# Optimization experiments

Measured on AMD Instinct MI355X. Metric: run time of the kernel, lower is better.

The kernel has to match this reference:

```python
import jax, jax.numpy as jnp
import numpy as np

SEGMENT_LENGTHS = [2048, 4096, 8192]
DILATION_RATES = [1, 2, 4]
RING_SIZE = 4


def _head_groups(h, g):
    base, rem = divmod(h, g)
    return [base + (1 if i < rem else 0) for i in range(g)]


def _dilation_pattern(n, seg, r, group_idx):
    # Per-segment dilated index pattern of total length n (index_select target).
    s = min(seg, n)
    off = group_idx % r
    base = (off + np.arange(0, s, r)) % s          # stride-r indices within segment
    pat_seg = np.tile(base, r)[:s]                  # repeat to fill segment length
    nseg = n // s
    pat = (pat_seg[None, :] + np.arange(nseg)[:, None] * s).reshape(-1)
    return pat


def _apply_dilation(x):
    # x: (b, n, h, d). Gather along sequence per head group.
    b, n, h, d = x.shape
    groups = _head_groups(h, len(SEGMENT_LENGTHS))
    outs, hs = [], 0
    for i, (seg, r, g) in enumerate(zip(SEGMENT_LENGTHS, DILATION_RATES, groups)):
        if g == 0:
            continue
        pat = jnp.asarray(_dilation_pattern(n, seg, r, i))
        outs.append(x[:, pat, hs:hs + g, :])
        hs += g
    return jnp.concatenate(outs, axis=2)


def setup_inputs() -> dict:
    key = jax.random.key(0)
    k1, k2, k3 = jax.random.split(key, 3)
    shape = (1, 8192, 16, 64)
    return {
        "q": jax.random.normal(k1, shape, dtype=jnp.float32),
        "k": jax.random.normal(k2, shape, dtype=jnp.float32),
        "v": jax.random.normal(k3, shape, dtype=jnp.float32),
    }


def reference(q, k, v):
    b, n, h, d = q.shape
    scale = 1.0 / jnp.sqrt(jnp.asarray(d, q.dtype))
    chunk = n // RING_SIZE

    # Dilate queries once; dilate each local KV chunk (ring-distributed layout).
    qt = _apply_dilation(q).transpose(0, 2, 1, 3)   # (b, h, n, d)

    acc_out = jnp.zeros((b, h, n, d), q.dtype)
    acc_lse = jnp.full((b, h, n), -jnp.inf, q.dtype)

    # Simulated ring pass: iterate over KV chunks with online-LSE accumulation.
    for c in range(RING_SIZE):
        kc = _apply_dilation(k[:, c * chunk:(c + 1) * chunk])  # (b, chunk, h, d)
        vc = _apply_dilation(v[:, c * chunk:(c + 1) * chunk])
        scores = jnp.einsum('bhqd,bkhd->bhqk', qt, kc) * scale
        lse_c = jax.nn.logsumexp(scores, axis=-1)              # (b, h, n)
        out_c = jnp.einsum('bhqk,bkhd->bhqd',
                           jax.nn.softmax(scores, axis=-1), vc)
        new_lse = jnp.logaddexp(acc_lse, lse_c)
        w_old = jnp.exp(acc_lse - new_lse)[..., None]
        w_new = jnp.exp(lse_c - new_lse)[..., None]
        acc_out = w_old * acc_out + w_new * out_c
        acc_lse = new_lse

    return acc_out.transpose(0, 2, 1, 3)  # (b, n, h, d)
```

## Files before the change

### kernel.cpp

```cpp
#include <hip/hip_runtime.h>
#include <hip/hip_bf16.h>
#include <math.h>

typedef __attribute__((ext_vector_type(4))) float f32x4;
typedef __attribute__((ext_vector_type(8))) short bf16x8;
typedef __attribute__((ext_vector_type(4))) short s16x4;

#define NH 16
#define HD 64
#define BM 128
#define BN 64
#define WM 32
#define LDS_K 72
#define TILE_B 18432
#define TILE_S 9216
#define WS_NEEDED 23003136ull

__device__ __forceinline__ short f2bf(float f) {
    union { float f; unsigned u; } x; x.f = f;
    unsigned r = x.u + 0x7fffu + ((x.u >> 16) & 1u);
    return (short)(r >> 16);
}
__device__ __forceinline__ unsigned pack2bf(float a, float b) {
    union { float f; unsigned u; } x, y; x.f = a; y.f = b;
    return __builtin_amdgcn_perm(y.u + 0x8000u, x.u + 0x8000u, 0x07060302u);
}
__device__ __forceinline__ float elem(const float4& r, int j) {
    return ((const float*)&r)[j];
}
__device__ __forceinline__ size_t head_base(int h) {
    if (h < 6)  return (size_t)h * (128 * TILE_B);
    if (h < 11) return 6ull * (128 * TILE_B) + (size_t)(h - 6) * (64 * TILE_B);
    return 6ull * (128 * TILE_B) + 5ull * (64 * TILE_B) + (size_t)(h - 11) * (32 * TILE_B);
}

__global__ __launch_bounds__(256)
void rda_pack(const float* __restrict__ K, const float* __restrict__ V, char* __restrict__ W) {
    int bid = blockIdx.x;
    int h, t, type;
    if (bid < 768)       { type = 0; h = bid >> 7;                t = bid & 127; }
    else if (bid < 1088) { type = 1; h = 6 + ((bid - 768) >> 6);  t = (bid - 768) & 63; }
    else                 { type = 2; h = 11 + ((bid - 1088) >> 5); t = (bid - 1088) & 31; }
    int rate = 1 << type, off = type;
    char* tile = W + head_base(h) + (size_t)t * TILE_B;
    int tid = threadIdx.x;
    {
        int row = tid >> 2, c = (tid & 3) * 16;
        int pos = rate * (t * 64 + row) + off;
        const float* p = K + ((size_t)pos * NH + h) * HD + c;
        float4 a0 = ((const float4*)p)[0], a1 = ((const float4*)p)[1];
        float4 a2 = ((const float4*)p)[2], a3 = ((const float4*)p)[3];
        uint4 d0, d1;
        d0.x = pack2bf(elem(a0,0), elem(a0,1)); d0.y = pack2bf(elem(a0,2), elem(a0,3));
        d0.z = pack2bf(elem(a1,0), elem(a1,1)); d0.w = pack2bf(elem(a1,2), elem(a1,3));
        d1.x = pack2bf(elem(a2,0), elem(a2,1)); d1.y = pack2bf(elem(a2,2), elem(a2,3));
        d1.z = pack2bf(elem(a3,0), elem(a3,1)); d1.w = pack2bf(elem(a3,2), elem(a3,3));
        char* dst = tile + row * (LDS_K * 2) + c * 2;
        ((uint4*)dst)[0] = d0;
        ((uint4*)dst)[1] = d1;
    }
    {
        int vr = (tid & 15) * 4, vc = (tid >> 4) * 4;
        float4 vv[4];
#pragma unroll
        for (int i = 0; i < 4; ++i) {
            int pos = rate * (t * 64 + vr + i) + off;
            vv[i] = *(const float4*)(V + ((size_t)pos * NH + h) * HD + vc);
        }
#pragma unroll
        for (int j = 0; j < 4; ++j) {
            uint2 w;
            w.x = pack2bf(elem(vv[0], j), elem(vv[1], j));
            w.y = pack2bf(elem(vv[2], j), elem(vv[3], j));
            *(uint2*)(tile + 9216 + (vc + j) * (LDS_K * 2) + vr * 2) = w;
        }
    }
}

__global__ __launch_bounds__(256, 3)
void rda_attn(const float* __restrict__ Q, const char* __restrict__ W, float* __restrict__ O) {
    __shared__ __align__(16) short sKV[2 * TILE_S];
    __shared__ __align__(16) short sP[4][WM * 64];

    int bid = blockIdx.x;
    int h, mb, type;
    if (bid < 384)      { type = 0; h = bid >> 6;               mb = bid & 63; }
    else if (bid < 544) { type = 1; h = 6 + ((bid - 384) >> 5); mb = (bid - 384) & 31; }
    else                { type = 2; h = 11 + ((bid - 544) >> 4); mb = (bid - 544) & 15; }
    int rate = 1 << type;
    int off  = type;
    int nsteps = 128 >> type;

    int tid  = threadIdx.x;
    int wave = tid >> 6;
    int lane = tid & 63;
    int ln   = lane & 15;
    int quad = lane >> 4;

    const float SC = 0.125f * 1.4426950408889634f;

    int qbase = mb * BM + wave * WM;
    bf16x8 qf[2][2];
#pragma unroll
    for (int mt = 0; mt < 2; ++mt) {
        int u = qbase + mt * 16 + ln;
        size_t base = ((size_t)(rate * u + off) * NH + h) * HD;
#pragma unroll
        for (int ks = 0; ks < 2; ++ks) {
            const float* p = Q + base + ks * 32 + quad * 8;
            float4 a = ((const float4*)p)[0];
            float4 b = ((const float4*)p)[1];
            union { uint4 u4; bf16x8 f; } cv;
            cv.u4.x = pack2bf(elem(a,0)*SC, elem(a,1)*SC);
            cv.u4.y = pack2bf(elem(a,2)*SC, elem(a,3)*SC);
            cv.u4.z = pack2bf(elem(b,0)*SC, elem(b,1)*SC);
            cv.u4.w = pack2bf(elem(b,2)*SC, elem(b,3)*SC);
            qf[mt][ks] = cv.f;
        }
    }

    f32x4 acc[2][4];
#pragma unroll
    for (int mt = 0; mt < 2; ++mt)
#pragma unroll
        for (int dt = 0; dt < 4; ++dt) acc[mt][dt] = (f32x4){0.f, 0.f, 0.f, 0.f};
    float lp[2] = {0.f, 0.f};

    const char* gh = W + head_base(h);

    auto stage = [&](const char* gt, int lB) {
#pragma unroll
        for (int r = 0; r < 4; ++r) {
            int c = r * 4096 + tid * 16;
            __builtin_amdgcn_global_load_lds(
                (const __attribute__((address_space(1))) unsigned*)(gt + c),
                (__attribute__((address_space(3))) unsigned*)((char*)sKV + lB + c),
                16, 0, 0);
        }
        if (tid < 128) {
            int c = 16384 + tid * 16;
            __builtin_amdgcn_global_load_lds(
                (const __attribute__((address_space(1))) unsigned*)(gt + c),
                (__attribute__((address_space(3))) unsigned*)((char*)sKV + lB + c),
                16, 0, 0);
        }
    };

    stage(gh, 0);
    int pB = 0;

    char* pbase = (char*)&sP[wave][0];

    for (int kb = 0; kb < nsteps; ++kb) {
        __syncthreads();

        if (kb + 1 < nsteps) stage(gh + (size_t)(kb + 1) * TILE_B, pB ^ TILE_B);

        const short* sK  = (const short*)((const char*)sKV + pB);
        const short* sVT = sK + BN * LDS_K;

        f32x4 st[4][2];
        __builtin_amdgcn_s_setprio(1);
#pragma unroll
        for (int kt = 0; kt < 4; ++kt) {
            bf16x8 a0 = *(bf16x8*)&sK[(kt * 16 + ln) * LDS_K + quad * 8];
            bf16x8 a1 = *(bf16x8*)&sK[(kt * 16 + ln) * LDS_K + 32 + quad * 8];
#pragma unroll
            for (int mt = 0; mt < 2; ++mt) {
                f32x4 c = (f32x4){0.f, 0.f, 0.f, 0.f};
                c = __builtin_amdgcn_mfma_f32_16x16x32_bf16(a0, qf[mt][0], c, 0, 0, 0);
                c = __builtin_amdgcn_mfma_f32_16x16x32_bf16(a1, qf[mt][1], c, 0, 0, 0);
                st[kt][mt] = c;
            }
        }
        __builtin_amdgcn_s_setprio(0);

#pragma unroll
        for (int mt = 0; mt < 2; ++mt)
#pragma unroll
            for (int kt = 0; kt < 4; ++kt) {
                float p0 = __builtin_amdgcn_exp2f(st[kt][mt][0]);
                float p1 = __builtin_amdgcn_exp2f(st[kt][mt][1]);
                float p2 = __builtin_amdgcn_exp2f(st[kt][mt][2]);
                float p3 = __builtin_amdgcn_exp2f(st[kt][mt][3]);
                st[kt][mt][0] = p0; st[kt][mt][1] = p1;
                st[kt][mt][2] = p2; st[kt][mt][3] = p3;
                lp[mt] += (p0 + p1) + (p2 + p3);
            }

#pragma unroll
        for (int mt = 0; mt < 2; ++mt)
#pragma unroll
            for (int kt = 0; kt < 4; ++kt) {
                uint2 pk;
                pk.x = pack2bf(st[kt][mt][0], st[kt][mt][1]);
                pk.y = pack2bf(st[kt][mt][2], st[kt][mt][3]);
                int prow = mt * 16 + ln;
                int pbyte = (prow * 128 + (kt * 16 + quad * 4) * 2) ^ ((prow & 7) << 4);
                *(uint2*)(pbase + pbyte) = pk;
            }
        __asm__ volatile("s_waitcnt lgkmcnt(0)" ::: "memory");

        __builtin_amdgcn_s_setprio(1);
#pragma unroll
        for (int ksk = 0; ksk < 2; ++ksk) {
            int b0 = (ln * 128 + (ksk * 32 + quad * 8) * 2) ^ ((ln & 7) << 4);
            int b1 = ((16 + ln) * 128 + (ksk * 32 + quad * 8) * 2) ^ ((ln & 7) << 4);
            bf16x8 pa0 = *(bf16x8*)(pbase + b0);
            bf16x8 pa1 = *(bf16x8*)(pbase + b1);
#pragma unroll
            for (int dt = 0; dt < 4; ++dt) {
                bf16x8 vb = *(bf16x8*)&sVT[(dt * 16 + ln) * LDS_K + ksk * 32 + quad * 8];
                acc[0][dt] = __builtin_amdgcn_mfma_f32_16x16x32_bf16(pa0, vb, acc[0][dt], 0, 0, 0);
                acc[1][dt] = __builtin_amdgcn_mfma_f32_16x16x32_bf16(pa1, vb, acc[1][dt], 0, 0, 0);
            }
        }
        __builtin_amdgcn_s_setprio(0);
        pB ^= TILE_B;
    }

#pragma unroll
    for (int mt = 0; mt < 2; ++mt) {
        lp[mt] += __shfl_xor(lp[mt], 16);
        lp[mt] += __shfl_xor(lp[mt], 32);
#pragma unroll
        for (int r = 0; r < 4; ++r) {
            float lO = __shfl(lp[mt], quad * 4 + r);
            float inv = 1.0f / lO;
            int u = qbase + mt * 16 + quad * 4 + r;
#pragma unroll
            for (int dt = 0; dt < 4; ++dt) {
                float val = acc[mt][dt][r] * inv;
                int dcol = dt * 16 + ln;
                if (type == 0) {
                    O[((size_t)u * NH + h) * HD + dcol] = val;
                } else if (type == 1) {
                    int r0 = ((u >> 11) << 12) + (u & 2047);
                    O[((size_t)r0 * NH + h) * HD + dcol] = val;
                    O[((size_t)(r0 + 2048) * NH + h) * HD + dcol] = val;
                } else {
#pragma unroll
                    for (int t = 0; t < 4; ++t)
                        O[((size_t)(u + t * 2048) * NH + h) * HD + dcol] = val;
                }
            }
        }
    }
}

__global__ __launch_bounds__(256, 2)
void rda_attn_fb(const float* __restrict__ Q, const float* __restrict__ K,
                 const float* __restrict__ V, float* __restrict__ O) {
    __shared__ short sK[BN * LDS_K];
    __shared__ short sVT[HD * LDS_K];
    __shared__ short sP[4][WM * LDS_K];

    int bid = blockIdx.x;
    int h, mb, type;
    if (bid < 384)      { type = 0; h = bid >> 6;               mb = bid & 63; }
    else if (bid < 544) { type = 1; h = 6 + ((bid - 384) >> 5); mb = (bid - 384) & 31; }
    else                { type = 2; h = 11 + ((bid - 544) >> 4); mb = (bid - 544) & 15; }
    int rate = 1 << type;
    int off  = type;
    int nsteps = 128 >> type;

    int tid  = threadIdx.x;
    int wave = tid >> 6;
    int lane = tid & 63;
    int ln   = lane & 15;
    int quad = lane >> 4;

    const float SC = 0.125f * 1.4426950408889634f;

    int qbase = mb * BM + wave * WM;
    bf16x8 qf[2][2];
#pragma unroll
    for (int mt = 0; mt < 2; ++mt) {
        int u = qbase + mt * 16 + ln;
        size_t base = ((size_t)(rate * u + off) * NH + h) * HD;
#pragma unroll
        for (int ks = 0; ks < 2; ++ks) {
            const float* p = Q + base + ks * 32 + quad * 8;
            float4 a = ((const float4*)p)[0];
            float4 b = ((const float4*)p)[1];
            bf16x8 f;
#pragma unroll
            for (int i = 0; i < 4; ++i) { f[i] = f2bf(elem(a, i) * SC); f[4 + i] = f2bf(elem(b, i) * SC); }
            qf[mt][ks] = f;
        }
    }

    f32x4 acc[2][4];
#pragma unroll
    for (int mt = 0; mt < 2; ++mt)
#pragma unroll
        for (int dt = 0; dt < 4; ++dt) acc[mt][dt] = (f32x4){0.f, 0.f, 0.f, 0.f};
    float m_i[2] = {-INFINITY, -INFINITY};
    float l_i[2] = {0.f, 0.f};

    int srow = tid >> 2, sc0 = (tid & 3) * 16;
    int vr = (tid >> 4) * 4, vc = (tid & 15) * 4;

    for (int kb = 0; kb < nsteps; ++kb) {
        {
            int kpos = rate * (kb * BN + srow) + off;
            const float* p = K + ((size_t)kpos * NH + h) * HD + sc0;
            float4 kv0 = ((const float4*)p)[0], kv1 = ((const float4*)p)[1];
            float4 kv2 = ((const float4*)p)[2], kv3 = ((const float4*)p)[3];
            bf16x8 f0, f1;
#pragma unroll
            for (int i = 0; i < 4; ++i) {
                f0[i] = f2bf(elem(kv0, i)); f0[4 + i] = f2bf(elem(kv1, i));
                f1[i] = f2bf(elem(kv2, i)); f1[4 + i] = f2bf(elem(kv3, i));
            }
            *(bf16x8*)&sK[srow * LDS_K + sc0] = f0;
            *(bf16x8*)&sK[srow * LDS_K + sc0 + 8] = f1;
        }
        {
            float4 vv[4];
#pragma unroll
            for (int i = 0; i < 4; ++i) {
                int kpos = rate * (kb * BN + vr + i) + off;
                vv[i] = *(const float4*)(V + ((size_t)kpos * NH + h) * HD + vc);
            }
#pragma unroll
            for (int j = 0; j < 4; ++j) {
                s16x4 t;
                t[0] = f2bf(elem(vv[0], j)); t[1] = f2bf(elem(vv[1], j));
                t[2] = f2bf(elem(vv[2], j)); t[3] = f2bf(elem(vv[3], j));
                *(s16x4*)&sVT[(vc + j) * LDS_K + vr] = t;
            }
        }
        __syncthreads();

        f32x4 st[4][2];
#pragma unroll
        for (int kt = 0; kt < 4; ++kt) {
            bf16x8 a0 = *(bf16x8*)&sK[(kt * 16 + ln) * LDS_K + quad * 8];
            bf16x8 a1 = *(bf16x8*)&sK[(kt * 16 + ln) * LDS_K + 32 + quad * 8];
#pragma unroll
            for (int mt = 0; mt < 2; ++mt) {
                f32x4 c = (f32x4){0.f, 0.f, 0.f, 0.f};
                c = __builtin_amdgcn_mfma_f32_16x16x32_bf16(a0, qf[mt][0], c, 0, 0, 0);
                c = __builtin_amdgcn_mfma_f32_16x16x32_bf16(a1, qf[mt][1], c, 0, 0, 0);
                st[kt][mt] = c;
            }
        }

#pragma unroll
        for (int mt = 0; mt < 2; ++mt) {
            float tmax = -INFINITY;
#pragma unroll
            for (int kt = 0; kt < 4; ++kt)
#pragma unroll
                for (int r = 0; r < 4; ++r) tmax = fmaxf(tmax, st[kt][mt][r]);
            tmax = fmaxf(tmax, __shfl_xor(tmax, 16));
            tmax = fmaxf(tmax, __shfl_xor(tmax, 32));
            float mnew = fmaxf(m_i[mt], tmax);
            float al = exp2f(m_i[mt] - mnew);
            m_i[mt] = mnew;
            float rs = 0.f;
#pragma unroll
            for (int kt = 0; kt < 4; ++kt)
#pragma unroll
                for (int r = 0; r < 4; ++r) {
                    float pe = exp2f(st[kt][mt][r] - mnew);
                    st[kt][mt][r] = pe;
                    rs += pe;
                }
            rs += __shfl_xor(rs, 16);
            rs += __shfl_xor(rs, 32);
            l_i[mt] = l_i[mt] * al + rs;
#pragma unroll
            for (int r = 0; r < 4; ++r) {
                float aO = __shfl(al, quad * 4 + r);
#pragma unroll
                for (int dt = 0; dt < 4; ++dt) acc[mt][dt][r] *= aO;
            }
        }

#pragma unroll
        for (int mt = 0; mt < 2; ++mt)
#pragma unroll
            for (int kt = 0; kt < 4; ++kt) {
                s16x4 pk;
                pk[0] = f2bf(st[kt][mt][0]); pk[1] = f2bf(st[kt][mt][1]);
                pk[2] = f2bf(st[kt][mt][2]); pk[3] = f2bf(st[kt][mt][3]);
                *(s16x4*)&sP[wave][(mt * 16 + ln) * LDS_K + kt * 16 + quad * 4] = pk;
            }
        __asm__ volatile("s_waitcnt lgkmcnt(0)" ::: "memory");

#pragma unroll
        for (int ksk = 0; ksk < 2; ++ksk) {
            bf16x8 pa0 = *(bf16x8*)&sP[wave][(ln) * LDS_K + ksk * 32 + quad * 8];
            bf16x8 pa1 = *(bf16x8*)&sP[wave][(16 + ln) * LDS_K + ksk * 32 + quad * 8];
#pragma unroll
            for (int dt = 0; dt < 4; ++dt) {
                bf16x8 vb = *(bf16x8*)&sVT[(dt * 16 + ln) * LDS_K + ksk * 32 + quad * 8];
                acc[0][dt] = __builtin_amdgcn_mfma_f32_16x16x32_bf16(pa0, vb, acc[0][dt], 0, 0, 0);
                acc[1][dt] = __builtin_amdgcn_mfma_f32_16x16x32_bf16(pa1, vb, acc[1][dt], 0, 0, 0);
            }
        }
        __syncthreads();
    }

#pragma unroll
    for (int mt = 0; mt < 2; ++mt) {
#pragma unroll
        for (int r = 0; r < 4; ++r) {
            float lO = __shfl(l_i[mt], quad * 4 + r);
            float inv = 1.0f / lO;
            int u = qbase + mt * 16 + quad * 4 + r;
#pragma unroll
            for (int dt = 0; dt < 4; ++dt) {
                float val = acc[mt][dt][r] * inv;
                int dcol = dt * 16 + ln;
                if (type == 0) {
                    O[((size_t)u * NH + h) * HD + dcol] = val;
                } else if (type == 1) {
                    int r0 = ((u >> 11) << 12) + (u & 2047);
                    O[((size_t)r0 * NH + h) * HD + dcol] = val;
                    O[((size_t)(r0 + 2048) * NH + h) * HD + dcol] = val;
                } else {
#pragma unroll
                    for (int t = 0; t < 4; ++t)
                        O[((size_t)(u + t * 2048) * NH + h) * HD + dcol] = val;
                }
            }
        }
    }
}

extern "C" void kernel_launch(void* const* d_in, const int* in_sizes, int n_in,
                              void* d_out, int out_size, void* d_ws, size_t ws_size,
                              hipStream_t stream) {
    (void)in_sizes; (void)n_in; (void)out_size;
    const float* q = (const float*)d_in[0];
    const float* k = (const float*)d_in[1];
    const float* v = (const float*)d_in[2];
    float* o = (float*)d_out;
    if (ws_size >= WS_NEEDED && d_ws != nullptr) {
        rda_pack<<<dim3(1248), dim3(256), 0, stream>>>(k, v, (char*)d_ws);
        rda_attn<<<dim3(624), dim3(256), 0, stream>>>(q, (const char*)d_ws, o);
    } else {
        rda_attn_fb<<<dim3(624), dim3(256), 0, stream>>>(q, k, v, o);
    }
}
```

Before: 327.6 us.

## Split KV range across two blocks for heavy heads and combine partials

Adds a split-K attention kernel in which rate-1 and rate-2 heads divide their KV steps between two blocks. Each block writes an unnormalised partial output and row sum to workspace, and a new combine kernel adds the partials and normalises. The goal is to balance the uneven per-block work (128 steps versus 32) and fill more CUs. The cost is an extra kernel launch and partial-buffer traffic, and the path runs only when the workspace is large enough.

```diff
diff --git a/kernel.cpp b/kernel.cpp
--- a/kernel.cpp
+++ b/kernel.cpp
@@ -15,6 +15,11 @@
 #define TILE_B 18432
 #define TILE_S 9216
 #define WS_NEEDED 23003136ull
+
+#define NSPLIT 1088
+#define OPART_OFF 23003136ull
+#define LPART_OFF (OPART_OFF + 35651584ull)
+#define WS2_NEEDED (LPART_OFF + 557056ull)
 
 __device__ __forceinline__ short f2bf(float f) {
     union { float f; unsigned u; } x; x.f = f;
@@ -78,18 +83,18 @@
 }
 
 __global__ __launch_bounds__(256, 3)
-void rda_attn(const float* __restrict__ Q, const char* __restrict__ W, float* __restrict__ O) {
+void rda_attn_ks(const float* __restrict__ Q, char* __restrict__ W, float* __restrict__ O) {
     __shared__ __align__(16) short sKV[2 * TILE_S];
     __shared__ __align__(16) short sP[4][WM * 64];
 
     int bid = blockIdx.x;
-    int h, mb, type;
-    if (bid < 384)      { type = 0; h = bid >> 6;               mb = bid & 63; }
-    else if (bid < 544) { type = 1; h = 6 + ((bid - 384) >> 5); mb = (bid - 384) & 31; }
-    else                { type = 2; h = 11 + ((bid - 544) >> 4); mb = (bid - 544) & 15; }
+    int h, mb, type, kc, nst, sid;
+    if (bid < 768)       { type = 0; h = bid >> 7; int rem = bid & 127; mb = rem >> 1; kc = rem & 1; nst = 64; sid = bid; }
+    else if (bid < 1088) { type = 1; int rel = bid - 768; h = 6 + (rel >> 6); int rem = rel & 63; mb = rem >> 1; kc = rem & 1; nst = 32; sid = bid; }
+    else                 { type = 2; int rel = bid - 1088; h = 11 + (rel >> 4); mb = rel & 15; kc = 0; nst = 32; sid = -1; }
     int rate = 1 << type;
     int off  = type;
-    int nsteps = 128 >> type;
+    int kb0  = kc * nst;
 
     int tid  = threadIdx.x;
     int wave = tid >> 6;
@@ -146,9 +151,229 @@
         }
     };
 
+    stage(gh + (size_t)kb0 * TILE_B, 0);
+    int pB = 0;
+
+    char* pbase = (char*)&sP[wave][0];
+
+    for (int i = 0; i < nst; ++i) {
+        int kb = kb0 + i;
+        __syncthreads();
+
+        if (i + 1 < nst) stage(gh + (size_t)(kb + 1) * TILE_B, pB ^ TILE_B);
+
+        const short* sK  = (const short*)((const char*)sKV + pB);
+        const short* sVT = sK + BN * LDS_K;
+
+        f32x4 st[4][2];
+        __builtin_amdgcn_s_setprio(1);
+#pragma unroll
+        for (int kt = 0; kt < 4; ++kt) {
+            bf16x8 a0 = *(bf16x8*)&sK[(kt * 16 + ln) * LDS_K + quad * 8];
+            bf16x8 a1 = *(bf16x8*)&sK[(kt * 16 + ln) * LDS_K + 32 + quad * 8];
+#pragma unroll
+            for (int mt = 0; mt < 2; ++mt) {
+                f32x4 c = (f32x4){0.f, 0.f, 0.f, 0.f};
+                c = __builtin_amdgcn_mfma_f32_16x16x32_bf16(a0, qf[mt][0], c, 0, 0, 0);
+                c = __builtin_amdgcn_mfma_f32_16x16x32_bf16(a1, qf[mt][1], c, 0, 0, 0);
+                st[kt][mt] = c;
+            }
+        }
+        __builtin_amdgcn_s_setprio(0);
+
+#pragma unroll
+        for (int mt = 0; mt < 2; ++mt)
+#pragma unroll
+            for (int kt = 0; kt < 4; ++kt) {
+                float p0 = __builtin_amdgcn_exp2f(st[kt][mt][0]);
+                float p1 = __builtin_amdgcn_exp2f(st[kt][mt][1]);
+                float p2 = __builtin_amdgcn_exp2f(st[kt][mt][2]);
+                float p3 = __builtin_amdgcn_exp2f(st[kt][mt][3]);
+                st[kt][mt][0] = p0; st[kt][mt][1] = p1;
+                st[kt][mt][2] = p2; st[kt][mt][3] = p3;
+                lp[mt] += (p0 + p1) + (p2 + p3);
+            }
+
+#pragma unroll
+        for (int mt = 0; mt < 2; ++mt)
+#pragma unroll
+            for (int kt = 0; kt < 4; ++kt) {
+                uint2 pk;
+                pk.x = pack2bf(st[kt][mt][0], st[kt][mt][1]);
+                pk.y = pack2bf(st[kt][mt][2], st[kt][mt][3]);
+                int prow = mt * 16 + ln;
+                int pbyte = (prow * 128 + (kt * 16 + quad * 4) * 2) ^ ((prow & 7) << 4);
+                *(uint2*)(pbase + pbyte) = pk;
+            }
+        __asm__ volatile("s_waitcnt lgkmcnt(0)" ::: "memory");
+
+        __builtin_amdgcn_s_setprio(1);
+#pragma unroll
+        for (int ksk = 0; ksk < 2; ++ksk) {
+            int b0 = (ln * 128 + (ksk * 32 + quad * 8) * 2) ^ ((ln & 7) << 4);
+            int b1 = ((16 + ln) * 128 + (ksk * 32 + quad * 8) * 2) ^ ((ln & 7) << 4);
+            bf16x8 pa0 = *(bf16x8*)(pbase + b0);
+            bf16x8 pa1 = *(bf16x8*)(pbase + b1);
+#pragma unroll
+            for (int dt = 0; dt < 4; ++dt) {
+                bf16x8 vb = *(bf16x8*)&sVT[(dt * 16 + ln) * LDS_K + ksk * 32 + quad * 8];
+                acc[0][dt] = __builtin_amdgcn_mfma_f32_16x16x32_bf16(pa0, vb, acc[0][dt], 0, 0, 0);
+                acc[1][dt] = __builtin_amdgcn_mfma_f32_16x16x32_bf16(pa1, vb, acc[1][dt], 0, 0, 0);
+            }
+        }
+        __builtin_amdgcn_s_setprio(0);
+        pB ^= TILE_B;
+    }
+
+#pragma unroll
+    for (int mt = 0; mt < 2; ++mt) {
+        lp[mt] += __shfl_xor(lp[mt], 16);
+        lp[mt] += __shfl_xor(lp[mt], 32);
+    }
+
+    if (type == 2) {
+#pragma unroll
+        for (int mt = 0; mt < 2; ++mt)
+#pragma unroll
+            for (int r = 0; r < 4; ++r) {
+                float lO = __shfl(lp[mt], quad * 4 + r);
+                float inv = 1.0f / lO;
+                int u = qbase + mt * 16 + quad * 4 + r;
+#pragma unroll
+                for (int dt = 0; dt < 4; ++dt) {
+                    float val = acc[mt][dt][r] * inv;
+                    int dcol = dt * 16 + ln;
+#pragma unroll
+                    for (int t = 0; t < 4; ++t)
+                        O[((size_t)(u + t * 2048) * NH + h) * HD + dcol] = val;
+                }
+            }
+    } else {
+        float* Op = (float*)(W + OPART_OFF) + (size_t)sid * (BM * HD);
+        float* Lp = (float*)(W + LPART_OFF) + (size_t)sid * BM;
+#pragma unroll
+        for (int mt = 0; mt < 2; ++mt) {
+            if (quad == 0) Lp[wave * WM + mt * 16 + ln] = lp[mt];
+#pragma unroll
+            for (int r = 0; r < 4; ++r) {
+                int ql = wave * WM + mt * 16 + quad * 4 + r;
+#pragma unroll
+                for (int dt = 0; dt < 4; ++dt)
+                    Op[ql * HD + dt * 16 + ln] = acc[mt][dt][r];
+            }
+        }
+    }
+}
+
+__global__ __launch_bounds__(256)
+void rda_comb(const char* __restrict__ W, float* __restrict__ O) {
+    int c = blockIdx.x;
+    int h, mb, type, s0;
+    if (c < 384) { type = 0; h = c >> 6;              mb = c & 63; s0 = c * 2; }
+    else         { type = 1; int rel = c - 384; h = 6 + (rel >> 5); mb = rel & 31; s0 = 768 + rel * 2; }
+
+    const float* P0 = (const float*)(W + OPART_OFF) + (size_t)s0 * (BM * HD);
+    const float* P1 = P0 + BM * HD;
+    const float* L0 = (const float*)(W + LPART_OFF) + (size_t)s0 * BM;
+    const float* L1 = L0 + BM;
+
+    __shared__ float sInv[BM];
+    int tid = threadIdx.x;
+    if (tid < BM) sInv[tid] = 1.0f / (L0[tid] + L1[tid]);
+    __syncthreads();
+
+#pragma unroll
+    for (int i = 0; i < 8; ++i) {
+        int f = i * 256 + tid;
+        int q = f >> 4, d4 = f & 15;
+        float4 a = ((const float4*)P0)[f];
+        float4 b = ((const float4*)P1)[f];
+        float inv = sInv[q];
+        float4 v;
+        v.x = (a.x + b.x) * inv; v.y = (a.y + b.y) * inv;
+        v.z = (a.z + b.z) * inv; v.w = (a.w + b.w) * inv;
+        int u = mb * BM + q;
+        if (type == 0) {
+            *(float4*)&O[((size_t)u * NH + h) * HD + d4 * 4] = v;
+        } else {
+            int r0 = ((u >> 11) << 12) + (u & 2047);
+            *(float4*)&O[((size_t)r0 * NH + h) * HD + d4 * 4] = v;
+            *(float4*)&O[((size_t)(r0 + 2048) * NH + h) * HD + d4 * 4] = v;
+        }
+    }
+}
+
+__global__ __launch_bounds__(256, 3)
+void rda_attn(const float* __restrict__ Q, const char* __restrict__ W, float* __restrict__ O) {
+    __shared__ __align__(16) short sKV[2 * TILE_S];
+    __shared__ __align__(16) short sP[4][WM * 64];
+
+    int bid = blockIdx.x;
+    int h, mb, type;
+    if (bid < 384)      { type = 0; h = bid >> 6;               mb = bid & 63; }
+    else if (bid < 544) { type = 1; h = 6 + ((bid - 384) >> 5); mb = (bid - 384) & 31; }
+    else                { type = 2; h = 11 + ((bid - 544) >> 4); mb = (bid - 544) & 15; }
+    int rate = 1 << type;
+    int off  = type;
+    int nsteps = 128 >> type;
+
+    int tid  = threadIdx.x;
+    int wave = tid >> 6;
+    int lane = tid & 63;
+    int ln   = lane & 15;
+    int quad = lane >> 4;
+
+    const float SC = 0.125f * 1.4426950408889634f;
+
+    int qbase = mb * BM + wave * WM;
+    bf16x8 qf[2][2];
+#pragma unroll
+    for (int mt = 0; mt < 2; ++mt) {
+        int u = qbase + mt * 16 + ln;
+        size_t base = ((size_t)(rate * u + off) * NH + h) * HD;
+#pragma unroll
+        for (int ks = 0; ks < 2; ++ks) {
+            const float* p = Q + base + ks * 32 + quad * 8;
+            float4 a = ((const float4*)p)[0];
+            float4 b = ((const float4*)p)[1];
+            union { uint4 u4; bf16x8 f; } cv;
+            cv.u4.x = pack2bf(elem(a,0)*SC, elem(a,1)*SC);
+            cv.u4.y = pack2bf(elem(a,2)*SC, elem(a,3)*SC);
+            cv.u4.z = pack2bf(elem(b,0)*SC, elem(b,1)*SC);
+            cv.u4.w = pack2bf(elem(b,2)*SC, elem(b,3)*SC);
+            qf[mt][ks] = cv.f;
+        }
+    }
+
+    f32x4 acc[2][4];
+#pragma unroll
+    for (int mt = 0; mt < 2; ++mt)
+#pragma unroll
+        for (int dt = 0; dt < 4; ++dt) acc[mt][dt] = (f32x4){0.f, 0.f, 0.f, 0.f};
+    float lp[2] = {0.f, 0.f};
+
+    const char* gh = W + head_base(h);
+
+    auto stage = [&](const char* gt, int lB) {
+#pragma unroll
+        for (int r = 0; r < 4; ++r) {
+            int c = r * 4096 + tid * 16;
+            __builtin_amdgcn_global_load_lds(
+                (const __attribute__((address_space(1))) unsigned*)(gt + c),
+                (__attribute__((address_space(3))) unsigned*)((char*)sKV + lB + c),
+                16, 0, 0);
+        }
+        if (tid < 128) {
+            int c = 16384 + tid * 16;
+            __builtin_amdgcn_global_load_lds(
+                (const __attribute__((address_space(1))) unsigned*)(gt + c),
+                (__attribute__((address_space(3))) unsigned*)((char*)sKV + lB + c),
+                16, 0, 0);
+        }
+    };
+
     stage(gh, 0);
     int pB = 0;
-
     char* pbase = (char*)&sP[wave][0];
 
     for (int kb = 0; kb < nsteps; ++kb) {
@@ -439,7 +664,11 @@
     const float* k = (const float*)d_in[1];
     const float* v = (const float*)d_in[2];
     float* o = (float*)d_out;
-    if (ws_size >= WS_NEEDED && d_ws != nullptr) {
+    if (ws_size >= WS2_NEEDED && d_ws != nullptr) {
+        rda_pack<<<dim3(1248), dim3(256), 0, stream>>>(k, v, (char*)d_ws);
+        rda_attn_ks<<<dim3(1168), dim3(256), 0, stream>>>(q, (char*)d_ws, o);
+        rda_comb<<<dim3(544), dim3(256), 0, stream>>>((const char*)d_ws, o);
+    } else if (ws_size >= WS_NEEDED && d_ws != nullptr) {
         rda_pack<<<dim3(1248), dim3(256), 0, stream>>>(k, v, (char*)d_ws);
         rda_attn<<<dim3(624), dim3(256), 0, stream>>>(q, (const char*)d_ws, o);
     } else {
```

Result: faster. 303.3 us (-7.4%).

## Use 8-wave blocks with 256-row Q tiles and split-K for rate-1 heads

Applied to the files above, without the earlier changes.

The main attention kernel now runs 512-thread blocks covering 256 query rows, so each staged K/V tile is shared by twice as many waves. For the rate-1 heads, which have the longest key range, the key range is split in two across blocks. Those blocks write unnormalized partial outputs and row sums to workspace, and a new combine kernel adds the halves and normalizes. This trades a larger workspace, extra partial-output traffic and one more launch for more key/value reuse and better balance across heads. If the workspace is too small it falls back to the unchanged original path.

```diff
diff --git a/kernel.cpp b/kernel.cpp
--- a/kernel.cpp
+++ b/kernel.cpp
@@ -9,12 +9,16 @@
 #define NH 16
 #define HD 64
 #define BM 128
+#define BM2 256
 #define BN 64
 #define WM 32
 #define LDS_K 72
 #define TILE_B 18432
 #define TILE_S 9216
-#define WS_NEEDED 23003136ull
+
+#define OPART4_OFF 23003136ull
+#define LPART4_OFF (OPART4_OFF + 25165824ull)
+#define WS4_NEEDED (LPART4_OFF + 393216ull)
 
 __device__ __forceinline__ short f2bf(float f) {
     union { float f; unsigned u; } x; x.f = f;
@@ -77,19 +81,19 @@
     }
 }
 
-__global__ __launch_bounds__(256, 3)
-void rda_attn(const float* __restrict__ Q, const char* __restrict__ W, float* __restrict__ O) {
+__global__ __launch_bounds__(512, 4)
+void rda_attn_w8(const float* __restrict__ Q, char* __restrict__ W, float* __restrict__ O) {
     __shared__ __align__(16) short sKV[2 * TILE_S];
-    __shared__ __align__(16) short sP[4][WM * 64];
+    __shared__ __align__(16) short sP[8][WM * 64];
 
     int bid = blockIdx.x;
-    int h, mb, type;
-    if (bid < 384)      { type = 0; h = bid >> 6;               mb = bid & 63; }
-    else if (bid < 544) { type = 1; h = 6 + ((bid - 384) >> 5); mb = (bid - 384) & 31; }
-    else                { type = 2; h = 11 + ((bid - 544) >> 4); mb = (bid - 544) & 15; }
+    int h, mb, type, kc, nst, sid;
+    if (bid < 384)      { type = 0; h = bid >> 6; int rem = bid & 63; mb = rem >> 1; kc = rem & 1; nst = 64; sid = bid; }
+    else if (bid < 464) { type = 1; int rel = bid - 384; h = 6 + (rel >> 4); mb = rel & 15; kc = 0; nst = 64; sid = -1; }
+    else                { type = 2; int rel = bid - 464; h = 11 + (rel >> 3); mb = rel & 7; kc = 0; nst = 32; sid = -1; }
     int rate = 1 << type;
     int off  = type;
-    int nsteps = 128 >> type;
+    int kb0  = kc * 64;
 
     int tid  = threadIdx.x;
     int wave = tid >> 6;
@@ -99,7 +103,7 @@
 
     const float SC = 0.125f * 1.4426950408889634f;
 
-    int qbase = mb * BM + wave * WM;
+    int qbase = mb * BM2 + wave * WM;
     bf16x8 qf[2][2];
 #pragma unroll
     for (int mt = 0; mt < 2; ++mt) {
@@ -130,8 +134,8 @@
 
     auto stage = [&](const char* gt, int lB) {
 #pragma unroll
-        for (int r = 0; r < 4; ++r) {
-            int c = r * 4096 + tid * 16;
+        for (int r = 0; r < 2; ++r) {
+            int c = r * 8192 + tid * 16;
             __builtin_amdgcn_global_load_lds(
                 (const __attribute__((address_space(1))) unsigned*)(gt + c),
                 (__attribute__((address_space(3))) unsigned*)((char*)sKV + lB + c),
@@ -146,15 +150,16 @@
         }
     };
 
-    stage(gh, 0);
+    stage(gh + (size_t)kb0 * TILE_B, 0);
     int pB = 0;
 
     char* pbase = (char*)&sP[wave][0];
 
-    for (int kb = 0; kb < nsteps; ++kb) {
+    for (int i = 0; i < nst; ++i) {
+        int kb = kb0 + i;
         __syncthreads();
 
-        if (kb + 1 < nsteps) stage(gh + (size_t)(kb + 1) * TILE_B, pB ^ TILE_B);
+        if (i + 1 < nst) stage(gh + (size_t)(kb + 1) * TILE_B, pB ^ TILE_B);
 
         const short* sK  = (const short*)((const char*)sKV + pB);
         const short* sVT = sK + BN * LDS_K;
@@ -223,9 +228,238 @@
     for (int mt = 0; mt < 2; ++mt) {
         lp[mt] += __shfl_xor(lp[mt], 16);
         lp[mt] += __shfl_xor(lp[mt], 32);
+    }
+
+    if (type == 0) {
+        float* Op = (float*)(W + OPART4_OFF) + (size_t)sid * (BM2 * HD);
+        float* Lp = (float*)(W + LPART4_OFF) + (size_t)sid * BM2;
+#pragma unroll
+        for (int mt = 0; mt < 2; ++mt) {
+            if (quad == 0) Lp[wave * WM + mt * 16 + ln] = lp[mt];
+#pragma unroll
+            for (int r = 0; r < 4; ++r) {
+                int ql = wave * WM + mt * 16 + quad * 4 + r;
+#pragma unroll
+                for (int dt = 0; dt < 4; ++dt)
+                    Op[ql * HD + dt * 16 + ln] = acc[mt][dt][r];
+            }
+        }
+    } else {
+#pragma unroll
+        for (int mt = 0; mt < 2; ++mt)
+#pragma unroll
+            for (int r = 0; r < 4; ++r) {
+                float lO = __shfl(lp[mt], quad * 4 + r);
+                float inv = 1.0f / lO;
+                int u = qbase + mt * 16 + quad * 4 + r;
+#pragma unroll
+                for (int dt = 0; dt < 4; ++dt) {
+                    float val = acc[mt][dt][r] * inv;
+                    int dcol = dt * 16 + ln;
+                    if (type == 1) {
+                        int r0 = ((u >> 11) << 12) + (u & 2047);
+                        O[((size_t)r0 * NH + h) * HD + dcol] = val;
+                        O[((size_t)(r0 + 2048) * NH + h) * HD + dcol] = val;
+                    } else {
+#pragma unroll
+                        for (int t = 0; t < 4; ++t)
+                            O[((size_t)(u + t * 2048) * NH + h) * HD + dcol] = val;
+                    }
+                }
+            }
+    }
+}
+
+__global__ __launch_bounds__(256)
+void rda_comb4(const char* __restrict__ W, float* __restrict__ O) {
+    int c = blockIdx.x;
+    int h = c >> 5, mb = c & 31;
+    int s0 = c * 2;
+
+    const float* P0 = (const float*)(W + OPART4_OFF) + (size_t)s0 * (BM2 * HD);
+    const float* L0 = (const float*)(W + LPART4_OFF) + (size_t)s0 * BM2;
+
+    __shared__ float sInv[BM2];
+    int tid = threadIdx.x;
+    sInv[tid] = 1.0f / (L0[tid] + L0[BM2 + tid]);
+    __syncthreads();
+
+#pragma unroll
+    for (int i = 0; i < 16; ++i) {
+        int f = i * 256 + tid;
+        int q = f >> 4, d4 = f & 15;
+        float4 a = ((const float4*)P0)[f];
+        float4 b = ((const float4*)(P0 + BM2 * HD))[f];
+        float inv = sInv[q];
+        float4 v;
+        v.x = (a.x + b.x) * inv; v.y = (a.y + b.y) * inv;
+        v.z = (a.z + b.z) * inv; v.w = (a.w + b.w) * inv;
+        int u = mb * BM2 + q;
+        *(float4*)&O[((size_t)u * NH + h) * HD + d4 * 4] = v;
+    }
+}
+
+__global__ __launch_bounds__(256, 2)
+void rda_attn_fb(const float* __restrict__ Q, const float* __restrict__ K,
+                 const float* __restrict__ V, float* __restrict__ O) {
+    __shared__ short sK[BN * LDS_K];
+    __shared__ short sVT[HD * LDS_K];
+    __shared__ short sP[4][WM * LDS_K];
+
+    int bid = blockIdx.x;
+    int h, mb, type;
+    if (bid < 384)      { type = 0; h = bid >> 6;               mb = bid & 63; }
+    else if (bid < 544) { type = 1; h = 6 + ((bid - 384) >> 5); mb = (bid - 384) & 31; }
+    else                { type = 2; h = 11 + ((bid - 544) >> 4); mb = (bid - 544) & 15; }
+    int rate = 1 << type;
+    int off  = type;
+    int nsteps = 128 >> type;
+
+    int tid  = threadIdx.x;
+    int wave = tid >> 6;
+    int lane = tid & 63;
+    int ln   = lane & 15;
+    int quad = lane >> 4;
+
+    const float SC = 0.125f * 1.4426950408889634f;
+
+    int qbase = mb * BM + wave * WM;
+    bf16x8 qf[2][2];
+#pragma unroll
+    for (int mt = 0; mt < 2; ++mt) {
+        int u = qbase + mt * 16 + ln;
+        size_t base = ((size_t)(rate * u + off) * NH + h) * HD;
+#pragma unroll
+        for (int ks = 0; ks < 2; ++ks) {
+            const float* p = Q + base + ks * 32 + quad * 8;
+            float4 a = ((const float4*)p)[0];
+            float4 b = ((const float4*)p)[1];
+            bf16x8 f;
+#pragma unroll
+            for (int i = 0; i < 4; ++i) { f[i] = f2bf(elem(a, i) * SC); f[4 + i] = f2bf(elem(b, i) * SC); }
+            qf[mt][ks] = f;
+        }
+    }
+
+    f32x4 acc[2][4];
+#pragma unroll
+    for (int mt = 0; mt < 2; ++mt)
+#pragma unroll
+        for (int dt = 0; dt < 4; ++dt) acc[mt][dt] = (f32x4){0.f, 0.f, 0.f, 0.f};
+    float m_i[2] = {-INFINITY, -INFINITY};
+    float l_i[2] = {0.f, 0.f};
+
+    int srow = tid >> 2, sc0 = (tid & 3) * 16;
+    int vr = (tid >> 4) * 4, vc = (tid & 15) * 4;
+
+    for (int kb = 0; kb < nsteps; ++kb) {
+        {
+            int kpos = rate * (kb * BN + srow) + off;
+            const float* p = K + ((size_t)kpos * NH + h) * HD + sc0;
+            float4 kv0 = ((const float4*)p)[0], kv1 = ((const float4*)p)[1];
+            float4 kv2 = ((const float4*)p)[2], kv3 = ((const float4*)p)[3];
+            bf16x8 f0, f1;
+#pragma unroll
+            for (int i = 0; i < 4; ++i) {
+                f0[i] = f2bf(elem(kv0, i)); f0[4 + i] = f2bf(elem(kv1, i));
+                f1[i] = f2bf(elem(kv2, i)); f1[4 + i] = f2bf(elem(kv3, i));
+            }
+            *(bf16x8*)&sK[srow * LDS_K + sc0] = f0;
+            *(bf16x8*)&sK[srow * LDS_K + sc0 + 8] = f1;
+        }
+        {
+            float4 vv[4];
+#pragma unroll
+            for (int i = 0; i < 4; ++i) {
+                int kpos = rate * (kb * BN + vr + i) + off;
+                vv[i] = *(const float4*)(V + ((size_t)kpos * NH + h) * HD + vc);
+            }
+#pragma unroll
+            for (int j = 0; j < 4; ++j) {
+                s16x4 t;
+                t[0] = f2bf(elem(vv[0], j)); t[1] = f2bf(elem(vv[1], j));
+                t[2] = f2bf(elem(vv[2], j)); t[3] = f2bf(elem(vv[3], j));
+                *(s16x4*)&sVT[(vc + j) * LDS_K + vr] = t;
+            }
+        }
+        __syncthreads();
+
+        f32x4 st[4][2];
+#pragma unroll
+        for (int kt = 0; kt < 4; ++kt) {
+            bf16x8 a0 = *(bf16x8*)&sK[(kt * 16 + ln) * LDS_K + quad * 8];
+            bf16x8 a1 = *(bf16x8*)&sK[(kt * 16 + ln) * LDS_K + 32 + quad * 8];
+#pragma unroll
+            for (int mt = 0; mt < 2; ++mt) {
+                f32x4 c = (f32x4){0.f, 0.f, 0.f, 0.f};
+                c = __builtin_amdgcn_mfma_f32_16x16x32_bf16(a0, qf[mt][0], c, 0, 0, 0);
+                c = __builtin_amdgcn_mfma_f32_16x16x32_bf16(a1, qf[mt][1], c, 0, 0, 0);
+                st[kt][mt] = c;
+            }
+        }
+
+#pragma unroll
+        for (int mt = 0; mt < 2; ++mt) {
+            float tmax = -INFINITY;
+#pragma unroll
+            for (int kt = 0; kt < 4; ++kt)
+#pragma unroll
+                for (int r = 0; r < 4; ++r) tmax = fmaxf(tmax, st[kt][mt][r]);
+            tmax = fmaxf(tmax, __shfl_xor(tmax, 16));
+            tmax = fmaxf(tmax, __shfl_xor(tmax, 32));
+            float mnew = fmaxf(m_i[mt], tmax);
+            float al = exp2f(m_i[mt] - mnew);
+            m_i[mt] = mnew;
+            float rs = 0.f;
+#pragma unroll
+            for (int kt = 0; kt < 4; ++kt)
+#pragma unroll
+                for (int r = 0; r < 4; ++r) {
+                    float pe = exp2f(st[kt][mt][r] - mnew);
+                    st[kt][mt][r] = pe;
+                    rs += pe;
+                }
+            rs += __shfl_xor(rs, 16);
+            rs += __shfl_xor(rs, 32);
+            l_i[mt] = l_i[mt] * al + rs;
+#pragma unroll
+            for (int r = 0; r < 4; ++r) {
+                float aO = __shfl(al, quad * 4 + r);
+#pragma unroll
+                for (int dt = 0; dt < 4; ++dt) acc[mt][dt][r] *= aO;
+            }
+        }
+
+#pragma unroll
+        for (int mt = 0; mt < 2; ++mt)
+#pragma unroll
+            for (int kt = 0; kt < 4; ++kt) {
+                s16x4 pk;
+                pk[0] = f2bf(st[kt][mt][0]); pk[1] = f2bf(st[kt][mt][1]);
+                pk[2] = f2bf(st[kt][mt][2]); pk[3] = f2bf(st[kt][mt][3]);
+                *(s16x4*)&sP[wave][(mt * 16 + ln) * LDS_K + kt * 16 + quad * 4] = pk;
+            }
+        __asm__ volatile("s_waitcnt lgkmcnt(0)" ::: "memory");
+
+#pragma unroll
+        for (int ksk = 0; ksk < 2; ++ksk) {
+            bf16x8 pa0 = *(bf16x8*)&sP[wave][(ln) * LDS_K + ksk * 32 + quad * 8];
+            bf16x8 pa1 = *(bf16x8*)&sP[wave][(16 + ln) * LDS_K + ksk * 32 + quad * 8];
+#pragma unroll
+            for (int dt = 0; dt < 4; ++dt) {
+                bf16x8 vb = *(bf16x8*)&sVT[(dt * 16 + ln) * LDS_K + ksk * 32 + quad * 8];
+                acc[0][dt] = __builtin_amdgcn_mfma_f32_16x16x32_bf16(pa0, vb, acc[0][dt], 0, 0, 0);
+                acc[1][dt] = __builtin_amdgcn_mfma_f32_16x16x32_bf16(pa1, vb, acc[1][dt], 0, 0, 0);
+            }
+        }
+        __syncthreads();
+    }
+
+#pragma unroll
+    for (int mt = 0; mt < 2; ++mt) {
 #pragma unroll
         for (int r = 0; r < 4; ++r) {
-            float lO = __shfl(lp[mt], quad * 4 + r);
+            float lO = __shfl(l_i[mt], quad * 4 + r);
             float inv = 1.0f / lO;
             int u = qbase + mt * 16 + quad * 4 + r;
 #pragma unroll
@@ -248,189 +482,6 @@
     }
 }
 
-__global__ __launch_bounds__(256, 2)
-void rda_attn_fb(const float* __restrict__ Q, const float* __restrict__ K,
-                 const float* __restrict__ V, float* __restrict__ O) {
-    __shared__ short sK[BN * LDS_K];
-    __shared__ short sVT[HD * LDS_K];
-    __shared__ short sP[4][WM * LDS_K];
-
-    int bid = blockIdx.x;
-    int h, mb, type;
-    if (bid < 384)      { type = 0; h = bid >> 6;               mb = bid & 63; }
-    else if (bid < 544) { type = 1; h = 6 + ((bid - 384) >> 5); mb = (bid - 384) & 31; }
-    else                { type = 2; h = 11 + ((bid - 544) >> 4); mb = (bid - 544) & 15; }
-    int rate = 1 << type;
-    int off  = type;
-    int nsteps = 128 >> type;
-
-    int tid  = threadIdx.x;
-    int wave = tid >> 6;
-    int lane = tid & 63;
-    int ln   = lane & 15;
-    int quad = lane >> 4;
-
-    const float SC = 0.125f * 1.4426950408889634f;
-
-    int qbase = mb * BM + wave * WM;
-    bf16x8 qf[2][2];
-#pragma unroll
-    for (int mt = 0; mt < 2; ++mt) {
-        int u = qbase + mt * 16 + ln;
-        size_t base = ((size_t)(rate * u + off) * NH + h) * HD;
-#pragma unroll
-        for (int ks = 0; ks < 2; ++ks) {
-            const float* p = Q + base + ks * 32 + quad * 8;
-            float4 a = ((const float4*)p)[0];
-            float4 b = ((const float4*)p)[1];
-            bf16x8 f;
-#pragma unroll
-            for (int i = 0; i < 4; ++i) { f[i] = f2bf(elem(a, i) * SC); f[4 + i] = f2bf(elem(b, i) * SC); }
-            qf[mt][ks] = f;
-        }
-    }
-
-    f32x4 acc[2][4];
-#pragma unroll
-    for (int mt = 0; mt < 2; ++mt)
-#pragma unroll
-        for (int dt = 0; dt < 4; ++dt) acc[mt][dt] = (f32x4){0.f, 0.f, 0.f, 0.f};
-    float m_i[2] = {-INFINITY, -INFINITY};
-    float l_i[2] = {0.f, 0.f};
-
-    int srow = tid >> 2, sc0 = (tid & 3) * 16;
-    int vr = (tid >> 4) * 4, vc = (tid & 15) * 4;
-
-    for (int kb = 0; kb < nsteps; ++kb) {
-        {
-            int kpos = rate * (kb * BN + srow) + off;
-            const float* p = K + ((size_t)kpos * NH + h) * HD + sc0;
-            float4 kv0 = ((const float4*)p)[0], kv1 = ((const float4*)p)[1];
-            float4 kv2 = ((const float4*)p)[2], kv3 = ((const float4*)p)[3];
-            bf16x8 f0, f1;
-#pragma unroll
-            for (int i = 0; i < 4; ++i) {
-                f0[i] = f2bf(elem(kv0, i)); f0[4 + i] = f2bf(elem(kv1, i));
-                f1[i] = f2bf(elem(kv2, i)); f1[4 + i] = f2bf(elem(kv3, i));
-            }
-            *(bf16x8*)&sK[srow * LDS_K + sc0] = f0;
-            *(bf16x8*)&sK[srow * LDS_K + sc0 + 8] = f1;
-        }
-        {
-            float4 vv[4];
-#pragma unroll
-            for (int i = 0; i < 4; ++i) {
-                int kpos = rate * (kb * BN + vr + i) + off;
-                vv[i] = *(const float4*)(V + ((size_t)kpos * NH + h) * HD + vc);
-            }
-#pragma unroll
-            for (int j = 0; j < 4; ++j) {
-                s16x4 t;
-                t[0] = f2bf(elem(vv[0], j)); t[1] = f2bf(elem(vv[1], j));
-                t[2] = f2bf(elem(vv[2], j)); t[3] = f2bf(elem(vv[3], j));
-                *(s16x4*)&sVT[(vc + j) * LDS_K + vr] = t;
-            }
-        }
-        __syncthreads();
-
-        f32x4 st[4][2];
-#pragma unroll
-        for (int kt = 0; kt < 4; ++kt) {
-            bf16x8 a0 = *(bf16x8*)&sK[(kt * 16 + ln) * LDS_K + quad * 8];
-            bf16x8 a1 = *(bf16x8*)&sK[(kt * 16 + ln) * LDS_K + 32 + quad * 8];
-#pragma unroll
-            for (int mt = 0; mt < 2; ++mt) {
-                f32x4 c = (f32x4){0.f, 0.f, 0.f, 0.f};
-                c = __builtin_amdgcn_mfma_f32_16x16x32_bf16(a0, qf[mt][0], c, 0, 0, 0);
-                c = __builtin_amdgcn_mfma_f32_16x16x32_bf16(a1, qf[mt][1], c, 0, 0, 0);
-                st[kt][mt] = c;
-            }
-        }
-
-#pragma unroll
-        for (int mt = 0; mt < 2; ++mt) {
-            float tmax = -INFINITY;
-#pragma unroll
-            for (int kt = 0; kt < 4; ++kt)
-#pragma unroll
-                for (int r = 0; r < 4; ++r) tmax = fmaxf(tmax, st[kt][mt][r]);
-            tmax = fmaxf(tmax, __shfl_xor(tmax, 16));
-            tmax = fmaxf(tmax, __shfl_xor(tmax, 32));
-            float mnew = fmaxf(m_i[mt], tmax);
-            float al = exp2f(m_i[mt] - mnew);
-            m_i[mt] = mnew;
-            float rs = 0.f;
-#pragma unroll
-            for (int kt = 0; kt < 4; ++kt)
-#pragma unroll
-                for (int r = 0; r < 4; ++r) {
-                    float pe = exp2f(st[kt][mt][r] - mnew);
-                    st[kt][mt][r] = pe;
-                    rs += pe;
-                }
-            rs += __shfl_xor(rs, 16);
-            rs += __shfl_xor(rs, 32);
-            l_i[mt] = l_i[mt] * al + rs;
-#pragma unroll
-            for (int r = 0; r < 4; ++r) {
-                float aO = __shfl(al, quad * 4 + r);
-#pragma unroll
-                for (int dt = 0; dt < 4; ++dt) acc[mt][dt][r] *= aO;
-            }
-        }
-
-#pragma unroll
-        for (int mt = 0; mt < 2; ++mt)
-#pragma unroll
-            for (int kt = 0; kt < 4; ++kt) {
-                s16x4 pk;
-                pk[0] = f2bf(st[kt][mt][0]); pk[1] = f2bf(st[kt][mt][1]);
-                pk[2] = f2bf(st[kt][mt][2]); pk[3] = f2bf(st[kt][mt][3]);
-                *(s16x4*)&sP[wave][(mt * 16 + ln) * LDS_K + kt * 16 + quad * 4] = pk;
-            }
-        __asm__ volatile("s_waitcnt lgkmcnt(0)" ::: "memory");
-
-#pragma unroll
-        for (int ksk = 0; ksk < 2; ++ksk) {
-            bf16x8 pa0 = *(bf16x8*)&sP[wave][(ln) * LDS_K + ksk * 32 + quad * 8];
-            bf16x8 pa1 = *(bf16x8*)&sP[wave][(16 + ln) * LDS_K + ksk * 32 + quad * 8];
-#pragma unroll
-            for (int dt = 0; dt < 4; ++dt) {
-                bf16x8 vb = *(bf16x8*)&sVT[(dt * 16 + ln) * LDS_K + ksk * 32 + quad * 8];
-                acc[0][dt] = __builtin_amdgcn_mfma_f32_16x16x32_bf16(pa0, vb, acc[0][dt], 0, 0, 0);
-                acc[1][dt] = __builtin_amdgcn_mfma_f32_16x16x32_bf16(pa1, vb, acc[1][dt], 0, 0, 0);
-            }
-        }
-        __syncthreads();
-    }
-
-#pragma unroll
-    for (int mt = 0; mt < 2; ++mt) {
-#pragma unroll
-        for (int r = 0; r < 4; ++r) {
-            float lO = __shfl(l_i[mt], quad * 4 + r);
-            float inv = 1.0f / lO;
-            int u = qbase + mt * 16 + quad * 4 + r;
-#pragma unroll
-            for (int dt = 0; dt < 4; ++dt) {
-                float val = acc[mt][dt][r] * inv;
-                int dcol = dt * 16 + ln;
-                if (type == 0) {
-                    O[((size_t)u * NH + h) * HD + dcol] = val;
-                } else if (type == 1) {
-                    int r0 = ((u >> 11) << 12) + (u & 2047);
-                    O[((size_t)r0 * NH + h) * HD + dcol] = val;
-                    O[((size_t)(r0 + 2048) * NH + h) * HD + dcol] = val;
-                } else {
-#pragma unroll
-                    for (int t = 0; t < 4; ++t)
-                        O[((size_t)(u + t * 2048) * NH + h) * HD + dcol] = val;
-                }
-            }
-        }
-    }
-}
-
 extern "C" void kernel_launch(void* const* d_in, const int* in_sizes, int n_in,
                               void* d_out, int out_size, void* d_ws, size_t ws_size,
                               hipStream_t stream) {
@@ -439,9 +490,10 @@
     const float* k = (const float*)d_in[1];
     const float* v = (const float*)d_in[2];
     float* o = (float*)d_out;
-    if (ws_size >= WS_NEEDED && d_ws != nullptr) {
+    if (ws_size >= WS4_NEEDED && d_ws != nullptr) {
         rda_pack<<<dim3(1248), dim3(256), 0, stream>>>(k, v, (char*)d_ws);
-        rda_attn<<<dim3(624), dim3(256), 0, stream>>>(q, (const char*)d_ws, o);
+        rda_attn_w8<<<dim3(504), dim3(512), 0, stream>>>(q, (char*)d_ws, o);
+        rda_comb4<<<dim3(192), dim3(256), 0, stream>>>((const char*)d_ws, o);
     } else {
         rda_attn_fb<<<dim3(624), dim3(256), 0, stream>>>(q, k, v, o);
     }
```

New measurement: 286.3 us. 1.14x faster.
